# Performance work log

Measured on AMD Instinct MI355X. Metric: run time of the kernel, lower is better.

The kernel has to match this reference:

```python
import jax, jax.numpy as jnp
import numpy as np

N_HEADS = 16
NEG = -1e9


def setup_inputs() -> dict:
    key = jax.random.key(0)
    ks = jax.random.split(key, 6)
    B, S, D = 4, 2048, 2048
    scale = 1.0 / np.sqrt(D)
    x = jax.random.normal(ks[0], (B, S, D), dtype=jnp.float32)
    attention_mask = jax.random.randint(ks[1], (B, S), 0, 2, dtype=jnp.int32)
    w_q = jax.random.normal(ks[2], (D, D), dtype=jnp.float32) * scale
    w_k = jax.random.normal(ks[3], (D, D), dtype=jnp.float32) * scale
    w_v = jax.random.normal(ks[4], (D, D), dtype=jnp.float32) * scale
    w_o = jax.random.normal(ks[5], (D, D), dtype=jnp.float32) * scale
    return {"x": x, "attention_mask": attention_mask,
            "w_q": w_q, "w_k": w_k, "w_v": w_v, "w_o": w_o}


def reference(x, attention_mask, w_q, w_k, w_v, w_o):
    B, S, D = x.shape
    H = N_HEADS
    dk = D // H

    def split_heads(t):  # [B,S,D] -> [B,H,S,dk]
        return t.reshape(B, S, H, dk).transpose(0, 2, 1, 3)

    # torch nn.Linear: y = x @ W.T (no bias)
    q = split_heads(x @ w_q.T)
    k = split_heads(x @ w_k.T)
    v = split_heads(x @ w_v.T)

    scores = jnp.einsum('bhqd,bhkd->bhqk', q, k) / jnp.sqrt(jnp.float32(dk))
    # padding mask over keys: [B,1,1,S]
    pad = attention_mask[:, None, None, :] != 0
    scores = jnp.where(pad, scores, NEG)
    # causal mask
    causal = jnp.tril(jnp.ones((S, S), dtype=bool))
    scores = jnp.where(causal[None, None, :, :], scores, NEG)

    attn = jax.nn.softmax(scores, axis=-1)
    # dropout p=0.0 -> identity
    out = jnp.einsum('bhqk,bhkd->bhqd', attn, v)
    out = out.transpose(0, 2, 1, 3).reshape(B, S, D)
    return out @ w_o.T
```

## Files before the change

### kernel.cpp

```cpp
#include <hip/hip_runtime.h>

typedef __bf16 bf16;
typedef __bf16 bf16x4 __attribute__((ext_vector_type(4)));
typedef __bf16 bf16x8 __attribute__((ext_vector_type(8)));
typedef float f32x4 __attribute__((ext_vector_type(4)));

#define NEGF (-1e9f)

__device__ __forceinline__ void gload16(const void* g, void* l) {
  __builtin_amdgcn_global_load_lds(
      (__attribute__((address_space(1))) void*)(void*)g,
      (__attribute__((address_space(3))) void*)l, 16, 0, 0);
}

__global__ __launch_bounds__(256)
void prep_kernel(const float* __restrict__ x, const int* __restrict__ mask,
                 const float* __restrict__ wq, const float* __restrict__ wk,
                 const float* __restrict__ wv, const float* __restrict__ wo,
                 bf16* __restrict__ xb, bf16* __restrict__ wqb,
                 bf16* __restrict__ wkb, bf16* __restrict__ wvb,
                 bf16* __restrict__ wob, float* __restrict__ maskadd,
                 int* __restrict__ firstone)
{
  const float QS = 1.44269504f * 0.08838834764f;
  const size_t i = ((size_t)blockIdx.x * 256 + threadIdx.x) * 4;
  if (i < (size_t)16777216) {
    const float4 v = *(const float4*)&x[i];
    bf16x4 o4 = {(bf16)v.x, (bf16)v.y, (bf16)v.z, (bf16)v.w};
    *(bf16x4*)&xb[i] = o4;
  }
  if (i < (size_t)4194304) {
    float4 v = *(const float4*)&wq[i];
    bf16x4 o4 = {(bf16)(v.x * QS), (bf16)(v.y * QS), (bf16)(v.z * QS), (bf16)(v.w * QS)};
    *(bf16x4*)&wqb[i] = o4;
    v = *(const float4*)&wk[i];
    bf16x4 o5 = {(bf16)v.x, (bf16)v.y, (bf16)v.z, (bf16)v.w};
    *(bf16x4*)&wkb[i] = o5;
    v = *(const float4*)&wv[i];
    bf16x4 o6 = {(bf16)v.x, (bf16)v.y, (bf16)v.z, (bf16)v.w};
    *(bf16x4*)&wvb[i] = o6;
    v = *(const float4*)&wo[i];
    bf16x4 o7 = {(bf16)v.x, (bf16)v.y, (bf16)v.z, (bf16)v.w};
    *(bf16x4*)&wob[i] = o7;
  }
  if (i < (size_t)8192) {
    const int4 m4 = *(const int4*)&mask[i];
    float4 o4 = {m4.x ? 0.f : NEGF, m4.y ? 0.f : NEGF,
                 m4.z ? 0.f : NEGF, m4.w ? 0.f : NEGF};
    *(float4*)&maskadd[i] = o4;
  }
  if (blockIdx.x == 16383) {
    __shared__ int fm;
    for (int b = 0; b < 4; ++b) {
      if (threadIdx.x == 0) fm = 2048;
      __syncthreads();
      int lm = 2048;
      for (int s = threadIdx.x; s < 2048; s += 256)
        if (mask[(b << 11) + s] != 0) lm = min(lm, s);
      atomicMin(&fm, lm);
      __syncthreads();
      if (threadIdx.x == 0) firstone[b] = fm;
      __syncthreads();
    }
  }
}

__device__ __forceinline__ void gemm_core256(
    const bf16* __restrict__ A, const bf16* __restrict__ Bt, const int K,
    const int rowBase, const int colBase, f32x4 acc[8][4])
{
  __shared__ __align__(16) bf16 As[2][256 * 64];
  __shared__ __align__(16) bf16 Bs[2][256 * 64];

  const int t = threadIdx.x;
  const int lane = t & 63;
  const int w = t >> 6;
  const int mh = (w >> 2) << 7;
  const int nq = (w & 3) << 6;
  const int l15 = lane & 15;
  const int quad = lane >> 4;

  const int srow = t >> 3;
  const int scol = ((t & 7) ^ (srow & 7)) << 3;
  const int doff = (srow << 6) + ((t & 7) << 3);

  auto issueA = [&](int buf, int k0, int g) {
    gload16(&A[(size_t)(rowBase + (g << 6) + srow) * K + k0 + scol],
            &As[buf][(g << 12) + doff]);
  };
  auto issueB = [&](int buf, int k0, int g) {
    gload16(&Bt[(size_t)(colBase + (g << 6) + srow) * K + k0 + scol],
            &Bs[buf][(g << 12) + doff]);
  };

  issueB(0, 0, 0); issueB(0, 0, 2); issueB(0, 0, 1); issueB(0, 0, 3);
  issueA(0, 0, 0); issueA(0, 0, 2); issueA(0, 0, 1); issueA(0, 0, 3);

  const int NT = K >> 6;
  for (int tt = 0; tt < NT; ++tt) {
    const int cur = tt & 1;
    const int nxt = cur ^ 1;
    const int k1 = (tt + 1 < NT) ? ((tt + 1) << 6) : 0;

    asm volatile("s_waitcnt vmcnt(2)" ::: "memory");
    __builtin_amdgcn_s_barrier();
    asm volatile("" ::: "memory");
    issueB(nxt, k1, 0); issueB(nxt, k1, 2);

    bf16x8 b[4][2], a[4][2];
#pragma unroll
    for (int ni = 0; ni < 4; ++ni)
#pragma unroll
      for (int ks = 0; ks < 2; ++ks) {
        const int row = nq + (ni << 4) + l15;
        b[ni][ks] = *(const bf16x8*)&Bs[cur][(row << 6) + ((((ks << 2) + quad) ^ (row & 7)) << 3)];
      }
#pragma unroll
    for (int mi = 0; mi < 4; ++mi)
#pragma unroll
      for (int ks = 0; ks < 2; ++ks) {
        const int row = mh + (mi << 4) + l15;
        a[mi][ks] = *(const bf16x8*)&As[cur][(row << 6) + ((((ks << 2) + quad) ^ (row & 7)) << 3)];
      }
    __builtin_amdgcn_s_setprio(1);
#pragma unroll
    for (int ks = 0; ks < 2; ++ks)
#pragma unroll
      for (int mi = 0; mi < 4; ++mi)
#pragma unroll
        for (int ni = 0; ni < 4; ++ni)
          acc[mi][ni] = __builtin_amdgcn_mfma_f32_16x16x32_bf16(
              a[mi][ks], b[ni][ks], acc[mi][ni], 0, 0, 0);
    __builtin_amdgcn_s_setprio(0);
    issueB(nxt, k1, 1); issueB(nxt, k1, 3);

    asm volatile("s_waitcnt vmcnt(4)" ::: "memory");
    __builtin_amdgcn_s_barrier();
    asm volatile("" ::: "memory");
    issueA(nxt, k1, 0); issueA(nxt, k1, 2);
#pragma unroll
    for (int mi = 0; mi < 4; ++mi)
#pragma unroll
      for (int ks = 0; ks < 2; ++ks) {
        const int row = mh + 64 + (mi << 4) + l15;
        a[mi][ks] = *(const bf16x8*)&As[cur][(row << 6) + ((((ks << 2) + quad) ^ (row & 7)) << 3)];
      }
    __builtin_amdgcn_s_setprio(1);
#pragma unroll
    for (int ks = 0; ks < 2; ++ks)
#pragma unroll
      for (int mi = 0; mi < 4; ++mi)
#pragma unroll
        for (int ni = 0; ni < 4; ++ni)
          acc[mi + 4][ni] = __builtin_amdgcn_mfma_f32_16x16x32_bf16(
              a[mi][ks], b[ni][ks], acc[mi + 4][ni], 0, 0, 0);
    __builtin_amdgcn_s_setprio(0);
    issueA(nxt, k1, 1); issueA(nxt, k1, 3);
  }
  asm volatile("s_waitcnt vmcnt(0)" ::: "memory");
  __builtin_amdgcn_s_barrier();
  asm volatile("" ::: "memory");
}

__global__ __launch_bounds__(512, 2)
void qkv_gemm_kernel(const bf16* __restrict__ xb,
                     const bf16* __restrict__ wqb, const bf16* __restrict__ wkb,
                     const bf16* __restrict__ wvb,
                     bf16* __restrict__ qb, bf16* __restrict__ kb,
                     bf16* __restrict__ vtb)
{
  const int id = blockIdx.x;
  const int nid = ((id & 7) * 96) + (id >> 3);
  const int z = nid >> 8;
  const int rem = nid & 255;
  const int rowBase = (rem >> 3) << 8;
  const int colBase = (rem & 7) << 8;
  const bf16* Bt = (z == 0) ? wqb : (z == 1) ? wkb : wvb;
  bf16* dst = (z == 0) ? qb : (z == 1) ? kb : vtb;

  f32x4 acc[8][4];
#pragma unroll
  for (int mi = 0; mi < 8; ++mi)
#pragma unroll
    for (int ni = 0; ni < 4; ++ni)
#pragma unroll
      for (int r = 0; r < 4; ++r) acc[mi][ni][r] = 0.f;

  gemm_core256(xb, Bt, 2048, rowBase, colBase, acc);

  const int lane = threadIdx.x & 63;
  const int w = threadIdx.x >> 6;
  const int mh = (w >> 2) << 7;
  const int nq = (w & 3) << 6;
  const int l15 = lane & 15;
  const int quad = lane >> 4;
#pragma unroll
  for (int mi = 0; mi < 8; ++mi)
#pragma unroll
    for (int ni = 0; ni < 4; ++ni)
#pragma unroll
      for (int r = 0; r < 4; ++r) {
        const int row = rowBase + mh + (mi << 4) + (quad << 2) + r;
        const int col = colBase + nq + (ni << 4) + l15;
        const int b = row >> 11, s = row & 2047;
        const int h = col >> 7, d = col & 127;
        const bf16 v = (bf16)acc[mi][ni][r];
        if (z == 2) dst[((((b << 4) + h) << 7) + d) * 2048 + s] = v;
        else        dst[(((((b << 4) + h) << 11) + s) << 7) + d] = v;
      }
}

__global__ __launch_bounds__(512, 2)
void out_gemm_kernel(const bf16* __restrict__ attnb, const bf16* __restrict__ wob,
                     float* __restrict__ out)
{
  const int id = blockIdx.x;
  const int nid = ((id & 7) * 32) + (id >> 3);
  const int rowBase = (nid >> 3) << 8;
  const int colBase = (nid & 7) << 8;

  f32x4 acc[8][4];
#pragma unroll
  for (int mi = 0; mi < 8; ++mi)
#pragma unroll
    for (int ni = 0; ni < 4; ++ni)
#pragma unroll
      for (int r = 0; r < 4; ++r) acc[mi][ni][r] = 0.f;

  gemm_core256(attnb, wob, 2048, rowBase, colBase, acc);

  const int lane = threadIdx.x & 63;
  const int w = threadIdx.x >> 6;
  const int mh = (w >> 2) << 7;
  const int nq = (w & 3) << 6;
  const int l15 = lane & 15;
  const int quad = lane >> 4;
#pragma unroll
  for (int mi = 0; mi < 8; ++mi)
#pragma unroll
    for (int ni = 0; ni < 4; ++ni)
#pragma unroll
      for (int r = 0; r < 4; ++r) {
        const int row = rowBase + mh + (mi << 4) + (quad << 2) + r;
        const int col = colBase + nq + (ni << 4) + l15;
        out[((size_t)row << 11) + col] = acc[mi][ni][r];
      }
}

__global__ __launch_bounds__(256, 2)
void flash_kernel(const bf16* __restrict__ qb, const bf16* __restrict__ kb,
                  const bf16* __restrict__ vtb, const float* __restrict__ maskadd,
                  bf16* __restrict__ attnb)
{
  __shared__ __align__(16) bf16 Ks[64 * 128];
  __shared__ __align__(16) bf16 Vs[128 * 64];

  const int h = blockIdx.y, b = blockIdx.z;
  const int qt = (b & 1) ? (int)blockIdx.x : 15 - (int)blockIdx.x;
  const int t = threadIdx.x, lane = t & 63, w = t >> 6;
  const int quad = lane >> 4, l15 = lane & 15;
  const int bh = (b << 4) + h;
  const bf16* Qp = qb + (size_t)bh * (2048 * 128);
  const bf16* Kp = kb + (size_t)bh * (2048 * 128);
  const bf16* Vp = vtb + (size_t)bh * (128 * 2048);
  const int qrow0 = (qt << 7) + (w << 5);

  bf16x8 qf[2][4];
#pragma unroll
  for (int mi = 0; mi < 2; ++mi)
#pragma unroll
    for (int kk = 0; kk < 4; ++kk)
      qf[mi][kk] = *(const bf16x8*)&Qp[((qrow0 + (mi << 4) + l15) << 7) + (kk << 5) + (quad << 3)];

  f32x4 o[2][8];
  float lpart[2][4];
#pragma unroll
  for (int mi = 0; mi < 2; ++mi)
#pragma unroll
    for (int r = 0; r < 4; ++r) lpart[mi][r] = 0.f;
#pragma unroll
  for (int mi = 0; mi < 2; ++mi)
#pragma unroll
    for (int dj = 0; dj < 8; ++dj)
#pragma unroll
      for (int r = 0; r < 4; ++r) o[mi][dj][r] = 0.f;

  bf16* Pw = &Ks[w << 11];
  const int nkt = (qt << 1) + 2;
  for (int kt = 0; kt < nkt; ++kt) {
    __syncthreads();
#pragma unroll
    for (int i = 0; i < 4; ++i) {
      const int c = (i << 8) + t;
      const int row = c >> 4;
      const int col = ((c & 15) ^ (row & 15)) << 3;
      gload16(&Kp[(((kt << 6) + row) << 7) + col], &Ks[c << 3]);
    }
#pragma unroll
    for (int i = 0; i < 4; ++i) {
      const int c = (i << 8) + t;
      const int row = c >> 3;
      const int col = ((c & 7) ^ (row & 7)) << 3;
      gload16(&Vp[(row << 11) + (kt << 6) + col], &Vs[c << 3]);
    }
    __syncthreads();

    const bool skip = (kt << 6) > qrow0 + 31;
    f32x4 S[2][4];
    if (!skip) {
#pragma unroll
      for (int mi = 0; mi < 2; ++mi)
#pragma unroll
        for (int nj = 0; nj < 4; ++nj)
#pragma unroll
          for (int r = 0; r < 4; ++r) S[mi][nj][r] = 0.f;
#pragma unroll
      for (int kk = 0; kk < 4; ++kk) {
        bf16x8 kf[4];
#pragma unroll
        for (int nj = 0; nj < 4; ++nj) {
          const int key = (nj << 4) + l15;
          const int gd = (kk << 2) + quad;
          kf[nj] = *(const bf16x8*)&Ks[(key << 7) + ((gd ^ (key & 15)) << 3)];
        }
#pragma unroll
        for (int mi = 0; mi < 2; ++mi)
#pragma unroll
          for (int nj = 0; nj < 4; ++nj)
            S[mi][nj] = __builtin_amdgcn_mfma_f32_16x16x32_bf16(qf[mi][kk], kf[nj], S[mi][nj], 0, 0, 0);
      }
      float mv[4];
#pragma unroll
      for (int nj = 0; nj < 4; ++nj)
        mv[nj] = maskadd[(b << 11) + (kt << 6) + (nj << 4) + l15];
      const bool diag = ((kt << 6) + 63 > qrow0);
#pragma unroll
      for (int mi = 0; mi < 2; ++mi)
#pragma unroll
        for (int nj = 0; nj < 4; ++nj)
#pragma unroll
          for (int r = 0; r < 4; ++r) {
            float s = S[mi][nj][r] + mv[nj];
            if (diag) {
              const int key = (kt << 6) + (nj << 4) + l15;
              const int qrow = qrow0 + (mi << 4) + (quad << 2) + r;
              if (key > qrow) s += NEGF;
            }
            const float p = __builtin_amdgcn_exp2f(s);
            S[mi][nj][r] = p;
            lpart[mi][r] += p;
          }
    }
    __syncthreads();
    if (!skip) {
#pragma unroll
      for (int mi = 0; mi < 2; ++mi)
#pragma unroll
        for (int nj = 0; nj < 4; ++nj)
#pragma unroll
          for (int r = 0; r < 4; ++r) {
            const int row = (mi << 4) + (quad << 2) + r;
            const int col = (nj << 4) + l15;
            Pw[(row << 6) + ((((col >> 3) ^ (row & 7)) << 3) | (col & 7))] = (bf16)S[mi][nj][r];
          }
#pragma unroll
      for (int kk = 0; kk < 2; ++kk) {
        bf16x8 pf[2];
#pragma unroll
        for (int mi = 0; mi < 2; ++mi) {
          const int row = (mi << 4) + l15;
          pf[mi] = *(const bf16x8*)&Pw[(row << 6) + ((((kk << 2) + quad) ^ (row & 7)) << 3)];
        }
#pragma unroll
        for (int dj = 0; dj < 8; ++dj) {
          const int d = (dj << 4) + l15;
          const int gd = (kk << 2) + quad;
          const bf16x8 vf = *(const bf16x8*)&Vs[(d << 6) + ((gd ^ (d & 7)) << 3)];
#pragma unroll
          for (int mi = 0; mi < 2; ++mi)
            o[mi][dj] = __builtin_amdgcn_mfma_f32_16x16x32_bf16(pf[mi], vf, o[mi][dj], 0, 0, 0);
        }
      }
    }
  }

#pragma unroll
  for (int mi = 0; mi < 2; ++mi)
#pragma unroll
    for (int r = 0; r < 4; ++r) {
      float s = lpart[mi][r];
#pragma unroll
      for (int off = 1; off < 16; off <<= 1) s += __shfl_xor(s, off);
      const float inv = 1.0f / s;
      const int row = qrow0 + (mi << 4) + (quad << 2) + r;
#pragma unroll
      for (int dj = 0; dj < 8; ++dj) {
        const int d = (dj << 4) + l15;
        attnb[((size_t)((b << 11) + row) << 11) + (h << 7) + d] = (bf16)(o[mi][dj][r] * inv);
      }
    }
}

__global__ void mean_v_kernel(const bf16* __restrict__ vtb, float* __restrict__ meanv)
{
  const int row = blockIdx.x;
  float sum = 0.f;
  for (int s = threadIdx.x; s < 2048; s += 256)
    sum += (float)vtb[((size_t)row << 11) + s];
#pragma unroll
  for (int off = 1; off < 64; off <<= 1) sum += __shfl_xor(sum, off);
  __shared__ float part[4];
  if ((threadIdx.x & 63) == 0) part[threadIdx.x >> 6] = sum;
  __syncthreads();
  if (threadIdx.x == 0)
    meanv[row] = (part[0] + part[1] + part[2] + part[3]) * (1.0f / 2048.0f);
}

__global__ void fixup_kernel(const int* __restrict__ firstone,
                             const float* __restrict__ meanv,
                             bf16* __restrict__ attnb)
{
  const int b = blockIdx.x, h = blockIdx.y, d = threadIdx.x;
  const int f = firstone[b];
  const bf16 v = (bf16)meanv[(((b << 4) + h) << 7) + d];
  for (int s = 0; s < f; ++s)
    attnb[((size_t)((b << 11) + s) << 11) + (h << 7) + d] = v;
}

extern "C" void kernel_launch(void* const* d_in, const int* in_sizes, int n_in,
                              void* d_out, int out_size, void* d_ws, size_t ws_size,
                              hipStream_t stream)
{
  const float* x  = (const float*)d_in[0];
  const int* mask = (const int*)d_in[1];
  const float* wq = (const float*)d_in[2];
  const float* wk = (const float*)d_in[3];
  const float* wv = (const float*)d_in[4];
  const float* wo = (const float*)d_in[5];
  float* out = (float*)d_out;

  char* ws = (char*)d_ws;
  bf16* xb      = (bf16*)(ws + 0);
  bf16* wqb     = (bf16*)(ws + 33554432);
  bf16* wkb     = (bf16*)(ws + 41943040);
  bf16* wvb     = (bf16*)(ws + 50331648);
  bf16* wob     = (bf16*)(ws + 58720256);
  bf16* qb      = (bf16*)(ws + 67108864);
  bf16* kb      = (bf16*)(ws + 100663296);
  bf16* vtb     = (bf16*)(ws + 134217728);
  bf16* attnb   = (bf16*)(ws + 167772160);
  float* maskadd= (float*)(ws + 201326592);
  float* meanv  = (float*)(ws + 201359360);
  int* firstone = (int*)(ws + 201392128);

  prep_kernel<<<16384, 256, 0, stream>>>(x, mask, wq, wk, wv, wo,
                                         xb, wqb, wkb, wvb, wob, maskadd, firstone);
  qkv_gemm_kernel<<<768, 512, 0, stream>>>(xb, wqb, wkb, wvb, qb, kb, vtb);
  mean_v_kernel<<<8192, 256, 0, stream>>>(vtb, meanv);
  flash_kernel<<<dim3(16, 16, 4), 256, 0, stream>>>(qb, kb, vtb, maskadd, attnb);
  fixup_kernel<<<dim3(4, 16), 128, 0, stream>>>(firstone, meanv, attnb);
  out_gemm_kernel<<<256, 512, 0, stream>>>(attnb, wob, out);
}
```

Measured before the change: 689.7 us.

## Restructure GEMM core into eight-phase ping-pong schedule with half-tile LDS buffers

The shared GEMM core used by the QKV and output projections is rewritten to split A and B tiles into 128-row halves and to run an 8-phase loop covering two K-tiles. Each phase loads a small set of fragments, issues a slice of the next global-to-LDS loads, synchronises, then runs a short MFMA burst between barriers. The aim is to interleave memory traffic with matrix math more finely, in the style of the HipKittens 8-wave schedule. The cost is more barriers per K-step and tricky vmcnt accounting that could stall or race if it is wrong.

```diff
diff --git a/kernel.cpp b/kernel.cpp
--- a/kernel.cpp
+++ b/kernel.cpp
@@ -65,18 +65,54 @@
   }
 }
 
+#define GPHASE(d, q, VM, ...)                                                   \
+  {                                                                             \
+    if (q == 0) {                                                               \
+      _Pragma("unroll") for (int ni = 0; ni < 4; ++ni)                          \
+        _Pragma("unroll") for (int ks = 0; ks < 2; ++ks) {                      \
+          const int row = nq + (ni << 4) + l15;                                 \
+          bfr[ni][ks] = *(const bf16x8*)&Bs[d][hB][(row << 6) +                 \
+                        ((((ks << 2) + quad) ^ (row & 7)) << 3)];               \
+        }                                                                       \
+    }                                                                           \
+    bf16x8 afr[2][2];                                                           \
+    _Pragma("unroll") for (int mi = 0; mi < 2; ++mi)                            \
+      _Pragma("unroll") for (int ks = 0; ks < 2; ++ks) {                        \
+        const int row = (((q << 1) + mi) << 4) + l15;                           \
+        afr[mi][ks] = *(const bf16x8*)&As[d][hA][(row << 6) +                   \
+                      ((((ks << 2) + quad) ^ (row & 7)) << 3)];                 \
+      }                                                                         \
+    __VA_ARGS__;                                                                \
+    if (VM) asm volatile("s_waitcnt vmcnt(4)" ::: "memory");                    \
+    asm volatile("" ::: "memory");                                              \
+    __builtin_amdgcn_s_barrier();                                               \
+    asm volatile("s_waitcnt lgkmcnt(0)" ::: "memory");                          \
+    __builtin_amdgcn_s_setprio(1);                                              \
+    _Pragma("unroll") for (int ks = 0; ks < 2; ++ks)                            \
+      _Pragma("unroll") for (int mi = 0; mi < 2; ++mi)                          \
+        _Pragma("unroll") for (int ni = 0; ni < 4; ++ni)                        \
+          acc[(q << 1) + mi][ni] = __builtin_amdgcn_mfma_f32_16x16x32_bf16(     \
+              afr[mi][ks], bfr[ni][ks], acc[(q << 1) + mi][ni], 0, 0, 0);       \
+    __builtin_amdgcn_s_setprio(0);                                              \
+    asm volatile("" ::: "memory");                                              \
+    __builtin_amdgcn_s_barrier();                                               \
+    asm volatile("" ::: "memory");                                              \
+  }
+
 __device__ __forceinline__ void gemm_core256(
     const bf16* __restrict__ A, const bf16* __restrict__ Bt, const int K,
     const int rowBase, const int colBase, f32x4 acc[8][4])
 {
-  __shared__ __align__(16) bf16 As[2][256 * 64];
-  __shared__ __align__(16) bf16 Bs[2][256 * 64];
+  __shared__ __align__(16) bf16 As[2][2][128 * 64];
+  __shared__ __align__(16) bf16 Bs[2][2][128 * 64];
 
   const int t = threadIdx.x;
   const int lane = t & 63;
   const int w = t >> 6;
-  const int mh = (w >> 2) << 7;
-  const int nq = (w & 3) << 6;
+  const int hA = w >> 2;
+  const int bq = w & 3;
+  const int hB = bq >> 1;
+  const int nq = (bq & 1) << 6;
   const int l15 = lane & 15;
   const int quad = lane >> 4;
 
@@ -84,78 +120,39 @@
   const int scol = ((t & 7) ^ (srow & 7)) << 3;
   const int doff = (srow << 6) + ((t & 7) << 3);
 
-  auto issueA = [&](int buf, int k0, int g) {
-    gload16(&A[(size_t)(rowBase + (g << 6) + srow) * K + k0 + scol],
-            &As[buf][(g << 12) + doff]);
+  auto stA = [&](int d, int half, int kt) {
+#pragma unroll
+    for (int r = 0; r < 2; ++r)
+      gload16(&A[(size_t)(rowBase + (half << 7) + (r << 6) + srow) * K + (kt << 6) + scol],
+              &As[d][half][(r << 12) + doff]);
   };
-  auto issueB = [&](int buf, int k0, int g) {
-    gload16(&Bt[(size_t)(colBase + (g << 6) + srow) * K + k0 + scol],
-            &Bs[buf][(g << 12) + doff]);
+  auto stB = [&](int d, int half, int kt) {
+#pragma unroll
+    for (int r = 0; r < 2; ++r)
+      gload16(&Bt[(size_t)(colBase + (half << 7) + (r << 6) + srow) * K + (kt << 6) + scol],
+              &Bs[d][half][(r << 12) + doff]);
   };
 
-  issueB(0, 0, 0); issueB(0, 0, 2); issueB(0, 0, 1); issueB(0, 0, 3);
-  issueA(0, 0, 0); issueA(0, 0, 2); issueA(0, 0, 1); issueA(0, 0, 3);
+  stB(0, 0, 0); stB(0, 1, 0); stA(0, 0, 0); stA(0, 1, 0);
+  stB(1, 0, 1); stB(1, 1, 1);
+  asm volatile("s_waitcnt vmcnt(4)" ::: "memory");
+  __builtin_amdgcn_s_barrier();
+  asm volatile("" ::: "memory");
 
   const int NT = K >> 6;
-  for (int tt = 0; tt < NT; ++tt) {
-    const int cur = tt & 1;
-    const int nxt = cur ^ 1;
-    const int k1 = (tt + 1 < NT) ? ((tt + 1) << 6) : 0;
-
-    asm volatile("s_waitcnt vmcnt(2)" ::: "memory");
-    __builtin_amdgcn_s_barrier();
-    asm volatile("" ::: "memory");
-    issueB(nxt, k1, 0); issueB(nxt, k1, 2);
-
-    bf16x8 b[4][2], a[4][2];
-#pragma unroll
-    for (int ni = 0; ni < 4; ++ni)
-#pragma unroll
-      for (int ks = 0; ks < 2; ++ks) {
-        const int row = nq + (ni << 4) + l15;
-        b[ni][ks] = *(const bf16x8*)&Bs[cur][(row << 6) + ((((ks << 2) + quad) ^ (row & 7)) << 3)];
-      }
-#pragma unroll
-    for (int mi = 0; mi < 4; ++mi)
-#pragma unroll
-      for (int ks = 0; ks < 2; ++ks) {
-        const int row = mh + (mi << 4) + l15;
-        a[mi][ks] = *(const bf16x8*)&As[cur][(row << 6) + ((((ks << 2) + quad) ^ (row & 7)) << 3)];
-      }
-    __builtin_amdgcn_s_setprio(1);
-#pragma unroll
-    for (int ks = 0; ks < 2; ++ks)
-#pragma unroll
-      for (int mi = 0; mi < 4; ++mi)
-#pragma unroll
-        for (int ni = 0; ni < 4; ++ni)
-          acc[mi][ni] = __builtin_amdgcn_mfma_f32_16x16x32_bf16(
-              a[mi][ks], b[ni][ks], acc[mi][ni], 0, 0, 0);
-    __builtin_amdgcn_s_setprio(0);
-    issueB(nxt, k1, 1); issueB(nxt, k1, 3);
-
-    asm volatile("s_waitcnt vmcnt(4)" ::: "memory");
-    __builtin_amdgcn_s_barrier();
-    asm volatile("" ::: "memory");
-    issueA(nxt, k1, 0); issueA(nxt, k1, 2);
-#pragma unroll
-    for (int mi = 0; mi < 4; ++mi)
-#pragma unroll
-      for (int ks = 0; ks < 2; ++ks) {
-        const int row = mh + 64 + (mi << 4) + l15;
-        a[mi][ks] = *(const bf16x8*)&As[cur][(row << 6) + ((((ks << 2) + quad) ^ (row & 7)) << 3)];
-      }
-    __builtin_amdgcn_s_setprio(1);
-#pragma unroll
-    for (int ks = 0; ks < 2; ++ks)
-#pragma unroll
-      for (int mi = 0; mi < 4; ++mi)
-#pragma unroll
-        for (int ni = 0; ni < 4; ++ni)
-          acc[mi + 4][ni] = __builtin_amdgcn_mfma_f32_16x16x32_bf16(
-              a[mi][ks], b[ni][ks], acc[mi + 4][ni], 0, 0, 0);
-    __builtin_amdgcn_s_setprio(0);
-    issueA(nxt, k1, 1); issueA(nxt, k1, 3);
+  bf16x8 bfr[4][2];
+  for (int it = 0; it < (NT >> 1); ++it) {
+    const int t1 = (it << 1) + 1;
+    const int s2 = (t1 + 1 < NT) ? t1 + 1 : 0;
+    const int s3 = (t1 + 2 < NT) ? t1 + 2 : 0;
+    GPHASE(0, 0, false, stA(1, 0, t1); stA(1, 1, t1))
+    GPHASE(0, 1, false, )
+    GPHASE(0, 2, false, stB(0, 0, s2))
+    GPHASE(0, 3, true,  stB(0, 1, s2))
+    GPHASE(1, 0, false, stA(0, 0, s2))
+    GPHASE(1, 1, false, stA(0, 1, s2))
+    GPHASE(1, 2, false, stB(1, 0, s3))
+    GPHASE(1, 3, true,  stB(1, 1, s3))
   }
   asm volatile("s_waitcnt vmcnt(0)" ::: "memory");
   __builtin_amdgcn_s_barrier();
@@ -191,7 +188,7 @@
   const int lane = threadIdx.x & 63;
   const int w = threadIdx.x >> 6;
   const int mh = (w >> 2) << 7;
-  const int nq = (w & 3) << 6;
+  const int nqf = (w & 3) << 6;
   const int l15 = lane & 15;
   const int quad = lane >> 4;
 #pragma unroll
@@ -201,7 +198,7 @@
 #pragma unroll
       for (int r = 0; r < 4; ++r) {
         const int row = rowBase + mh + (mi << 4) + (quad << 2) + r;
-        const int col = colBase + nq + (ni << 4) + l15;
+        const int col = colBase + nqf + (ni << 4) + l15;
         const int b = row >> 11, s = row & 2047;
         const int h = col >> 7, d = col & 127;
         const bf16 v = (bf16)acc[mi][ni][r];
@@ -232,7 +229,7 @@
   const int lane = threadIdx.x & 63;
   const int w = threadIdx.x >> 6;
   const int mh = (w >> 2) << 7;
-  const int nq = (w & 3) << 6;
+  const int nqf = (w & 3) << 6;
   const int l15 = lane & 15;
   const int quad = lane >> 4;
 #pragma unroll
@@ -242,7 +239,7 @@
 #pragma unroll
       for (int r = 0; r < 4; ++r) {
         const int row = rowBase + mh + (mi << 4) + (quad << 2) + r;
-        const int col = colBase + nq + (ni << 4) + l15;
+        const int col = colBase + nqf + (ni << 4) + l15;
         out[((size_t)row << 11) + col] = acc[mi][ni][r];
       }
 }
```

New measurement: 669.4 us. -2.9%, faster.
